# Kernel optimization log

Measured on AMD Instinct MI355X. Metric: run time of the kernel, lower is better.

## Reference

```python
import jax, jax.numpy as jnp
import numpy as np

INPUT_SIZE = 1024
HIDDEN_SIZE = 1024
BATCH = 8192
MLP_H1, MLP_H2 = 16, 8


def _uniform(key, shape, stdv):
    return jax.random.uniform(key, shape, jnp.float32, -stdv, stdv)


def setup_inputs() -> dict:
    key = jax.random.key(0)
    ks = jax.random.split(key, 20)
    stdv = 1.0 / np.sqrt(HIDDEN_SIZE)
    I, H = INPUT_SIZE, HIDDEN_SIZE
    inp = {
        "x": jax.random.normal(ks[0], (BATCH, I), jnp.float32),
        "h": jax.random.normal(ks[1], (BATCH, H), jnp.float32),
        "c": jax.random.normal(ks[2], (BATCH, H), jnp.float32),
        # gate weights (torch layout: matmul(h, W_h*) + matmul(x, W_x*) + b)
        "W_hi": _uniform(ks[3], (H, H), stdv),
        "W_xi": _uniform(ks[4], (I, H), stdv),
        "b_i": _uniform(ks[5], (H,), stdv),
        "W_hc": _uniform(ks[6], (H, H), stdv),
        "W_xc": _uniform(ks[7], (I, H), stdv),
        "b_c": _uniform(ks[8], (H,), stdv),
        "W_ho": _uniform(ks[9], (H, H), stdv),
        "W_xo": _uniform(ks[10], (I, H), stdv),
        "b_o": _uniform(ks[11], (H,), stdv),
        # forget MLP: (I+H) -> 16 -> 8 -> H, ReLU hidden, sigmoid output
        "W1": _uniform(ks[12], (I + H, MLP_H1), stdv),
        "b1": _uniform(ks[13], (MLP_H1,), stdv),
        "W2": _uniform(ks[14], (MLP_H1, MLP_H2), stdv),
        "b2": _uniform(ks[15], (MLP_H2,), stdv),
        "W3": _uniform(ks[16], (MLP_H2, H), stdv),
        "b3": _uniform(ks[17], (H,), stdv),
    }
    return inp


def reference(x, h, c, W_hi, W_xi, b_i, W_hc, W_xc, b_c, W_ho, W_xo, b_o,
              W1, b1, W2, b2, W3, b3):
    # forget gate via small MLP on concat(x, h)
    xh = jnp.concatenate((x, h), axis=1)           # [B, I+H]
    z = jax.nn.relu(xh @ W1 + b1)                  # [B, 16]
    z = jax.nn.relu(z @ W2 + b2)                   # [B, 8]
    f = jax.nn.sigmoid(z @ W3 + b3)                # [B, H]

    i = jax.nn.sigmoid(h @ W_hi + x @ W_xi + b_i)
    g = jnp.tanh(h @ W_hc + x @ W_xc + b_c)
    o = jax.nn.sigmoid(h @ W_ho + x @ W_xo + b_o)

    c_new = f * c + i * g
    h_new = o * jnp.tanh(c_new)
    return (h_new, c_new, f)
```

## Files before the change

kernel.cpp:

```cpp
#include <hip/hip_runtime.h>
#include <math.h>

#define BATCH 8192
#define HDIM  1024
#define KDIM  2048
#define NDIM  3072

typedef __attribute__((ext_vector_type(8))) short short8;
typedef __attribute__((ext_vector_type(4))) float floatx4;

__device__ __forceinline__ float b2f(unsigned short u) {
  union { unsigned int i; float f; } v; v.i = ((unsigned int)u) << 16; return v.f;
}
__device__ __forceinline__ unsigned short f2b(float f) {
  union { unsigned int i; float f; } v; v.f = f;
  unsigned int r = v.i + 0x7FFFu + ((v.i >> 16) & 1u);
  return (unsigned short)(r >> 16);
}
__device__ __forceinline__ float ldsel(const void* p, size_t i, int isbf) {
  return isbf ? b2f(((const unsigned short*)p)[i]) : ((const float*)p)[i];
}
__device__ __forceinline__ float sigf(float x) { return 1.0f / (1.0f + __expf(-x)); }
__device__ __forceinline__ float tanhfast(float x) {
  float a = __builtin_fabsf(x);
  float t = __expf(-2.f * a);
  float r = (1.f - t) / (1.f + t);
  return copysignf(r, x);
}

__device__ __forceinline__ int detect_bf(const void* x) {
  unsigned int w = ((const unsigned int*)x)[threadIdx.x & 63];
  unsigned short lo = (unsigned short)(w & 0xFFFFu);
  int e = (lo >> 7) & 0xFF;
  bool ok = (e >= 110 && e <= 135) || ((lo & 0x7FFFu) == 0);
  unsigned long long m = __ballot(ok);
  return (__popcll(m) >= 48) ? 1 : 0;
}

__device__ __forceinline__ void gld16(const void* g, void* l) {
  auto gp = reinterpret_cast<__attribute__((address_space(1))) unsigned int*>(
      (unsigned long long)g);
  auto lp = reinterpret_cast<__attribute__((address_space(3))) unsigned int*>(
      (unsigned long long)l);
  __builtin_amdgcn_global_load_lds(gp, lp, 16, 0, 0);
}

__device__ __forceinline__ short8 ld8bf(const void* p, size_t off, int isbf) {
  short8 r;
  if (isbf) {
    r = *(const short8*)((const unsigned short*)p + off);
  } else {
    const float* s = (const float*)p + off;
    float4 a = *(const float4*)(s);
    float4 b = *(const float4*)(s + 4);
    r[0]=(short)f2b(a.x); r[1]=(short)f2b(a.y); r[2]=(short)f2b(a.z); r[3]=(short)f2b(a.w);
    r[4]=(short)f2b(b.x); r[5]=(short)f2b(b.y); r[6]=(short)f2b(b.z); r[7]=(short)f2b(b.w);
  }
  return r;
}

__global__ __launch_bounds__(256) void k_all(
    const void* __restrict__ x, const void* __restrict__ h,
    const void* __restrict__ wxi, const void* __restrict__ whi,
    const void* __restrict__ wxc, const void* __restrict__ whc,
    const void* __restrict__ wxo, const void* __restrict__ who,
    const void* __restrict__ W1, const void* __restrict__ b1,
    const void* __restrict__ W2, const void* __restrict__ b2,
    unsigned short* __restrict__ WT, unsigned short* __restrict__ A,
    float* __restrict__ z2) {
  __shared__ __align__(16) char smem[70976];
  const int isbf = detect_bf(x);
  const int bx = blockIdx.x;
  const int tid = threadIdx.x;

  if (bx < 512) {
    unsigned short* lW = (unsigned short*)smem;
    float* part = (float*)(smem + 65536);
    float* z1s  = (float*)(smem + 69888);
    const int m0 = bx * 16;
#pragma unroll
    for (int it = 0; it < 16; ++it) {
      const int chunk = it * 256 + tid;
      const int k = chunk >> 1;
      const int jh = (chunk & 1) * 8;
      unsigned short v[8];
      if (isbf) {
        short8 s = *(const short8*)((const unsigned short*)W1 + (size_t)k * 16 + jh);
#pragma unroll
        for (int j = 0; j < 8; ++j) v[j] = (unsigned short)s[j];
      } else {
        const float* s = (const float*)W1 + (size_t)k * 16 + jh;
        float4 a = *(const float4*)(s);
        float4 b = *(const float4*)(s + 4);
        v[0]=f2b(a.x); v[1]=f2b(a.y); v[2]=f2b(a.z); v[3]=f2b(a.w);
        v[4]=f2b(b.x); v[5]=f2b(b.y); v[6]=f2b(b.z); v[7]=f2b(b.w);
      }
#pragma unroll
      for (int j = 0; j < 8; ++j) {
        const int row = jh + j;
        lW[row * 2048 + (((k >> 3) ^ (row & 7)) << 3) + (k & 7)] = v[j];
      }
    }
    __syncthreads();
    const int w = tid >> 6;
    const int lane = tid & 63;
    const int q = lane >> 4;
    const int r = lane & 15;
    const void* src = (w >> 1) ? h : x;
    const size_t abase = (size_t)(m0 + r) * 1024 + (w & 1) * 512;
    const int kb = (w >> 1) * 1024 + (w & 1) * 512;
    floatx4 acc = {0.f, 0.f, 0.f, 0.f};
#pragma unroll 4
    for (int kt = 0; kt < 16; ++kt) {
      const int kl = kt * 32 + q * 8;
      short8 a = ld8bf(src, abase + kl, isbf);
      const int kg = kb + kl;
      short8 b = *(const short8*)(lW + r * 2048 + (((kg >> 3) ^ (r & 7)) << 3));
      acc = __builtin_amdgcn_mfma_f32_16x16x32_bf16(a, b, acc, 0, 0, 0);
    }
#pragma unroll
    for (int t = 0; t < 4; ++t) part[(w * 16 + q * 4 + t) * 17 + r] = acc[t];
    __syncthreads();
    {
      const int row = tid >> 4;
      const int n = tid & 15;
      float s = part[(0 * 16 + row) * 17 + n] + part[(1 * 16 + row) * 17 + n] +
                part[(2 * 16 + row) * 17 + n] + part[(3 * 16 + row) * 17 + n] +
                ldsel(b1, (size_t)n, isbf);
      z1s[row * 17 + n] = fmaxf(s, 0.f);
    }
    __syncthreads();
    if (tid < 128) {
      const int row = tid >> 3;
      const int p = tid & 7;
      float s = ldsel(b2, (size_t)p, isbf);
#pragma unroll
      for (int nn = 0; nn < 16; ++nn)
        s += z1s[row * 17 + nn] * ldsel(W2, (size_t)nn * 8 + p, isbf);
      z2[(size_t)(m0 + row) * 8 + p] = fmaxf(s, 0.f);
    }
  } else if (bx < 2048) {
    float (*tbuf)[65] = (float(*)[65])smem;
    const int b = bx - 512;
    const int mat = b >> 8;
    const int rem = b & 255;
    const int ti = rem >> 4;
    const int tj = rem & 15;
    const void* Ws[6] = {wxi, whi, wxc, whc, wxo, who};
    const void* W = Ws[mat];
    const int gt = mat >> 1;
    const int half = mat & 1;
    const int rrow = tid >> 3;
    const int c8 = (tid & 7) * 8;
#pragma unroll
    for (int it = 0; it < 2; ++it) {
      int row = it * 32 + rrow;
      size_t off = (size_t)(ti * 64 + row) * 1024 + tj * 64 + c8;
      if (isbf) {
        const unsigned short* s = (const unsigned short*)W + off;
        ushort4 a = *(const ushort4*)(s);
        ushort4 bv = *(const ushort4*)(s + 4);
        tbuf[row][c8+0]=b2f(a.x);  tbuf[row][c8+1]=b2f(a.y);
        tbuf[row][c8+2]=b2f(a.z);  tbuf[row][c8+3]=b2f(a.w);
        tbuf[row][c8+4]=b2f(bv.x); tbuf[row][c8+5]=b2f(bv.y);
        tbuf[row][c8+6]=b2f(bv.z); tbuf[row][c8+7]=b2f(bv.w);
      } else {
        const float* s = (const float*)W + off;
        float4 a = *(const float4*)(s);
        float4 bv = *(const float4*)(s + 4);
        tbuf[row][c8+0]=a.x;  tbuf[row][c8+1]=a.y;  tbuf[row][c8+2]=a.z;  tbuf[row][c8+3]=a.w;
        tbuf[row][c8+4]=bv.x; tbuf[row][c8+5]=bv.y; tbuf[row][c8+6]=bv.z; tbuf[row][c8+7]=bv.w;
      }
    }
    __syncthreads();
#pragma unroll
    for (int it = 0; it < 2; ++it) {
      int nl = it * 32 + rrow;
      int n = gt * 1024 + tj * 64 + nl;
      int kk = half * 1024 + ti * 64 + c8;
      short8 pk;
#pragma unroll
      for (int i = 0; i < 8; ++i) pk[i] = (short)f2b(tbuf[c8 + i][nl]);
      *(short8*)(WT + (size_t)n * KDIM + kk) = pk;
    }
  } else {
    if (isbf) return;
    size_t idx = ((size_t)(bx - 2048) * 256 + tid) * 8;
    int k = (int)(idx & 2047);
    size_t m = idx >> 11;
    const float* s = (k < 1024) ? (const float*)x + m * 1024 + k
                                : (const float*)h + m * 1024 + (k - 1024);
    float4 a = *(const float4*)(s);
    float4 b = *(const float4*)(s + 4);
    short8 pk;
    pk[0]=(short)f2b(a.x); pk[1]=(short)f2b(a.y); pk[2]=(short)f2b(a.z); pk[3]=(short)f2b(a.w);
    pk[4]=(short)f2b(b.x); pk[5]=(short)f2b(b.y); pk[6]=(short)f2b(b.z); pk[7]=(short)f2b(b.w);
    *(short8*)(A + idx) = pk;
  }
}

__global__ __launch_bounds__(256, 3) void k_gemm(
    const void* __restrict__ x, const void* __restrict__ h,
    const unsigned short* __restrict__ Apack,
    const unsigned short* __restrict__ WT,
    unsigned short* __restrict__ P) {
  const int isbf = detect_bf(x);
  const unsigned short* Ax = isbf ? (const unsigned short*)x : Apack;
  const unsigned short* Ah = isbf ? (const unsigned short*)h : (Apack + 1024);
  const int sA = isbf ? 1024 : 2048;
  __shared__ __align__(16) unsigned short lA[128 * 64];
  __shared__ __align__(16) unsigned short lB[128 * 64];
  const int tid = threadIdx.x;
  const int lane = tid & 63;
  const int wv = tid >> 6;
  const int wm = (wv >> 1) << 6;
  const int wn = (wv & 1) << 6;
  const int m0 = blockIdx.y << 7;
  const int n0 = blockIdx.x << 7;

  floatx4 acc[4][4];
  const floatx4 fzero = {0.f, 0.f, 0.f, 0.f};
#pragma unroll
  for (int i = 0; i < 4; ++i)
#pragma unroll
    for (int j = 0; j < 4; ++j) acc[i][j] = fzero;

  int rr[4], kk[4];
#pragma unroll
  for (int ps = 0; ps < 4; ++ps) {
    int chunk = ps * 256 + tid;
    rr[ps] = chunk >> 3;
    kk[ps] = (chunk & 7) ^ (rr[ps] & 7);
  }
  const int px0 = (lane >> 4) ^ (lane & 7);
  const int px1 = ((lane >> 4) + 4) ^ (lane & 7);
  const int rowA = wm + (lane & 15);
  const int rowB = wn + (lane & 15);

  for (int kt = 0; kt < KDIM / 64; ++kt) {
    const int k0 = kt * 64;
    const unsigned short* Abase = (k0 < 1024) ? (Ax + k0) : (Ah + (k0 - 1024));
#pragma unroll
    for (int ps = 0; ps < 4; ++ps) {
      const int chunk = ps * 256 + tid;
      gld16(Abase + (size_t)(m0 + rr[ps]) * sA + kk[ps] * 8, lA + chunk * 8);
      gld16(WT + ((size_t)(n0 + rr[ps]) * KDIM + k0 + kk[ps] * 8), lB + chunk * 8);
    }
    __syncthreads();
#pragma unroll
    for (int s = 0; s < 2; ++s) {
      const int px = s ? px1 : px0;
      short8 af[4], bfr[4];
#pragma unroll
      for (int i = 0; i < 4; ++i)
        af[i] = *(const short8*)(lA + ((((rowA + (i << 4)) << 3) + px) << 3));
#pragma unroll
      for (int i = 0; i < 4; ++i)
        bfr[i] = *(const short8*)(lB + ((((rowB + (i << 4)) << 3) + px) << 3));
#pragma unroll
      for (int mi = 0; mi < 4; ++mi)
#pragma unroll
        for (int ni = 0; ni < 4; ++ni)
          acc[mi][ni] = __builtin_amdgcn_mfma_f32_16x16x32_bf16(
              af[mi], bfr[ni], acc[mi][ni], 0, 0, 0);
    }
    __syncthreads();
  }
  const int col = lane & 15;
  const int rq = (lane >> 4) << 2;
#pragma unroll
  for (int mi = 0; mi < 4; ++mi) {
#pragma unroll
    for (int ni = 0; ni < 4; ++ni) {
      const size_t n = (size_t)(n0 + wn + (ni << 4) + col);
#pragma unroll
      for (int t = 0; t < 4; ++t) {
        const size_t m = (size_t)(m0 + wm + (mi << 4) + rq + t);
        P[m * NDIM + n] = f2b(acc[mi][ni][t]);
      }
    }
  }
}

__global__ __launch_bounds__(256) void k_pointwise(
    const unsigned short* __restrict__ P, const void* __restrict__ x,
    const void* __restrict__ cin,
    const void* __restrict__ bi, const void* __restrict__ bc,
    const void* __restrict__ bo, const float* __restrict__ z2,
    const void* __restrict__ W3, const void* __restrict__ b3,
    void* __restrict__ out) {
  const int isbf = detect_bf(x);
  __shared__ unsigned short w3s[8192];
  const int tid = threadIdx.x;
#pragma unroll
  for (int it = 0; it < 4; ++it) {
    const int idx = (it * 256 + tid) * 8;
    if (isbf) {
      *(short8*)(w3s + idx) = *(const short8*)((const unsigned short*)W3 + idx);
    } else {
      const float* s = (const float*)W3 + idx;
      float4 a = *(const float4*)(s);
      float4 b = *(const float4*)(s + 4);
      short8 pk;
      pk[0]=(short)f2b(a.x); pk[1]=(short)f2b(a.y); pk[2]=(short)f2b(a.z); pk[3]=(short)f2b(a.w);
      pk[4]=(short)f2b(b.x); pk[5]=(short)f2b(b.y); pk[6]=(short)f2b(b.z); pk[7]=(short)f2b(b.w);
      *(short8*)(w3s + idx) = pk;
    }
  }
  __syncthreads();
  const size_t MH = (size_t)BATCH * HDIM;
  const size_t m = blockIdx.x;
  const int n = tid * 4;
  const size_t idx = m * 1024 + n;
  const unsigned short* pr = P + m * NDIM + n;
  ushort4 ui = *(const ushort4*)(pr);
  ushort4 ug = *(const ushort4*)(pr + 1024);
  ushort4 uo = *(const ushort4*)(pr + 2048);
  float pi[4] = {b2f(ui.x), b2f(ui.y), b2f(ui.z), b2f(ui.w)};
  float pg[4] = {b2f(ug.x), b2f(ug.y), b2f(ug.z), b2f(ug.w)};
  float po[4] = {b2f(uo.x), b2f(uo.y), b2f(uo.z), b2f(uo.w)};
  float4 za = *(const float4*)(z2 + m * 8);
  float4 zb = *(const float4*)(z2 + m * 8 + 4);
  float zz[8] = {za.x, za.y, za.z, za.w, zb.x, zb.y, zb.z, zb.w};
  float f3[4];
  float bif[4], bcf[4], bof[4], cf[4];
  if (isbf) {
    ushort4 u3 = *(const ushort4*)((const unsigned short*)b3 + n);
    f3[0]=b2f(u3.x); f3[1]=b2f(u3.y); f3[2]=b2f(u3.z); f3[3]=b2f(u3.w);
    ushort4 a = *(const ushort4*)((const unsigned short*)bi + n);
    ushort4 b = *(const ushort4*)((const unsigned short*)bc + n);
    ushort4 d = *(const ushort4*)((const unsigned short*)bo + n);
    ushort4 e = *(const ushort4*)((const unsigned short*)cin + idx);
    bif[0]=b2f(a.x); bif[1]=b2f(a.y); bif[2]=b2f(a.z); bif[3]=b2f(a.w);
    bcf[0]=b2f(b.x); bcf[1]=b2f(b.y); bcf[2]=b2f(b.z); bcf[3]=b2f(b.w);
    bof[0]=b2f(d.x); bof[1]=b2f(d.y); bof[2]=b2f(d.z); bof[3]=b2f(d.w);
    cf[0]=b2f(e.x);  cf[1]=b2f(e.y);  cf[2]=b2f(e.z);  cf[3]=b2f(e.w);
  } else {
    float4 u3 = *(const float4*)((const float*)b3 + n);
    f3[0]=u3.x; f3[1]=u3.y; f3[2]=u3.z; f3[3]=u3.w;
    float4 a = *(const float4*)((const float*)bi + n);
    float4 b = *(const float4*)((const float*)bc + n);
    float4 d = *(const float4*)((const float*)bo + n);
    float4 e = *(const float4*)((const float*)cin + idx);
    bif[0]=a.x; bif[1]=a.y; bif[2]=a.z; bif[3]=a.w;
    bcf[0]=b.x; bcf[1]=b.y; bcf[2]=b.z; bcf[3]=b.w;
    bof[0]=d.x; bof[1]=d.y; bof[2]=d.z; bof[3]=d.w;
    cf[0]=e.x;  cf[1]=e.y;  cf[2]=e.z;  cf[3]=e.w;
  }
#pragma unroll
  for (int j = 0; j < 8; ++j) {
    const unsigned short* wr = w3s + j * 1024 + n;
    f3[0] += zz[j] * b2f(wr[0]);
    f3[1] += zz[j] * b2f(wr[1]);
    f3[2] += zz[j] * b2f(wr[2]);
    f3[3] += zz[j] * b2f(wr[3]);
  }
  float hn[4], cn[4], ff[4];
#pragma unroll
  for (int t = 0; t < 4; ++t) {
    float F = sigf(f3[t]);
    float I = sigf(pi[t] + bif[t]);
    float G = tanhfast(pg[t] + bcf[t]);
    float O = sigf(po[t] + bof[t]);
    float C = F * cf[t] + I * G;
    ff[t] = F;
    cn[t] = C;
    hn[t] = O * tanhfast(C);
  }
  if (isbf) {
    unsigned short* ob = (unsigned short*)out;
    *(ushort4*)(ob + idx) = make_ushort4(f2b(hn[0]), f2b(hn[1]), f2b(hn[2]), f2b(hn[3]));
    *(ushort4*)(ob + MH + idx) = make_ushort4(f2b(cn[0]), f2b(cn[1]), f2b(cn[2]), f2b(cn[3]));
    *(ushort4*)(ob + 2 * MH + idx) = make_ushort4(f2b(ff[0]), f2b(ff[1]), f2b(ff[2]), f2b(ff[3]));
  } else {
    float* ob = (float*)out;
    *(float4*)(ob + idx) = make_float4(hn[0], hn[1], hn[2], hn[3]);
    *(float4*)(ob + MH + idx) = make_float4(cn[0], cn[1], cn[2], cn[3]);
    *(float4*)(ob + 2 * MH + idx) = make_float4(ff[0], ff[1], ff[2], ff[3]);
  }
}

extern "C" void kernel_launch(void* const* d_in, const int* in_sizes, int n_in,
                              void* d_out, int out_size, void* d_ws, size_t ws_size,
                              hipStream_t stream) {
  const void* x    = d_in[0];
  const void* h    = d_in[1];
  const void* c    = d_in[2];
  const void* W_hi = d_in[3];
  const void* W_xi = d_in[4];
  const void* b_i  = d_in[5];
  const void* W_hc = d_in[6];
  const void* W_xc = d_in[7];
  const void* b_c  = d_in[8];
  const void* W_ho = d_in[9];
  const void* W_xo = d_in[10];
  const void* b_o  = d_in[11];
  const void* W1   = d_in[12];
  const void* b1   = d_in[13];
  const void* W2   = d_in[14];
  const void* b2   = d_in[15];
  const void* W3   = d_in[16];
  const void* b3   = d_in[17];

  char* ws = (char*)d_ws;
  unsigned short* A   = (unsigned short*)ws;
  unsigned short* WT  = (unsigned short*)(ws + 33554432);
  unsigned short* P   = (unsigned short*)(ws + 46137344);
  float*          z2b = (float*)(ws + 96468992);

  k_all<<<dim3(512 + 1536 + 8192), dim3(256), 0, stream>>>(
      x, h, W_xi, W_hi, W_xc, W_hc, W_xo, W_ho, W1, b_i ? b1 : b1, W2, b2,
      WT, A, z2b);
  k_gemm<<<dim3(NDIM / 128, BATCH / 128), dim3(256), 0, stream>>>(x, h, A, WT, P);
  k_pointwise<<<dim3(BATCH), dim3(256), 0, stream>>>(P, x, c, b_i, b_c, b_o,
                                                     z2b, W3, b3, d_out);
}
```

Before: 374.9 us.

## Split fused prep kernel into three kernels and register-cache W3 in pointwise

The monolithic prep kernel, which reserved about 70KB of shared memory for every block, is split into separate kernels for activation packing, weight transpose and the forget-gate MLP. Each can then run at its natural occupancy, and the transpose and packing blocks no longer carry the MLP's large LDS footprint. The pointwise kernel now processes 8 rows per block and keeps W3 and the biases in registers, removing the per-block LDS staging of W3. The costs are extra kernel launches and serialisation between the prep stages, plus higher register pressure in the pointwise kernel.

```diff
diff --git a/kernel.cpp b/kernel.cpp
--- a/kernel.cpp
+++ b/kernel.cpp
@@ -59,135 +59,144 @@
   return r;
 }
 
-__global__ __launch_bounds__(256) void k_all(
+__global__ __launch_bounds__(256) void k_z2(
     const void* __restrict__ x, const void* __restrict__ h,
+    const void* __restrict__ W1, const void* __restrict__ b1,
+    const void* __restrict__ W2, const void* __restrict__ b2,
+    float* __restrict__ z2) {
+  __shared__ __align__(16) char smem[70976];
+  const int isbf = detect_bf(x);
+  const int tid = threadIdx.x;
+  unsigned short* lW = (unsigned short*)smem;
+  float* part = (float*)(smem + 65536);
+  float* z1s  = (float*)(smem + 69888);
+  const int m0 = blockIdx.x * 16;
+#pragma unroll
+  for (int it = 0; it < 16; ++it) {
+    const int chunk = it * 256 + tid;
+    const int k = chunk >> 1;
+    const int jh = (chunk & 1) * 8;
+    unsigned short v[8];
+    if (isbf) {
+      short8 s = *(const short8*)((const unsigned short*)W1 + (size_t)k * 16 + jh);
+#pragma unroll
+      for (int j = 0; j < 8; ++j) v[j] = (unsigned short)s[j];
+    } else {
+      const float* s = (const float*)W1 + (size_t)k * 16 + jh;
+      float4 a = *(const float4*)(s);
+      float4 b = *(const float4*)(s + 4);
+      v[0]=f2b(a.x); v[1]=f2b(a.y); v[2]=f2b(a.z); v[3]=f2b(a.w);
+      v[4]=f2b(b.x); v[5]=f2b(b.y); v[6]=f2b(b.z); v[7]=f2b(b.w);
+    }
+#pragma unroll
+    for (int j = 0; j < 8; ++j) {
+      const int row = jh + j;
+      lW[row * 2048 + (((k >> 3) ^ (row & 7)) << 3) + (k & 7)] = v[j];
+    }
+  }
+  __syncthreads();
+  const int w = tid >> 6;
+  const int lane = tid & 63;
+  const int q = lane >> 4;
+  const int r = lane & 15;
+  const void* src = (w >> 1) ? h : x;
+  const size_t abase = (size_t)(m0 + r) * 1024 + (w & 1) * 512;
+  const int kb = (w >> 1) * 1024 + (w & 1) * 512;
+  floatx4 acc = {0.f, 0.f, 0.f, 0.f};
+#pragma unroll 4
+  for (int kt = 0; kt < 16; ++kt) {
+    const int kl = kt * 32 + q * 8;
+    short8 a = ld8bf(src, abase + kl, isbf);
+    const int kg = kb + kl;
+    short8 b = *(const short8*)(lW + r * 2048 + (((kg >> 3) ^ (r & 7)) << 3));
+    acc = __builtin_amdgcn_mfma_f32_16x16x32_bf16(a, b, acc, 0, 0, 0);
+  }
+#pragma unroll
+  for (int t = 0; t < 4; ++t) part[(w * 16 + q * 4 + t) * 17 + r] = acc[t];
+  __syncthreads();
+  {
+    const int row = tid >> 4;
+    const int n = tid & 15;
+    float s = part[(0 * 16 + row) * 17 + n] + part[(1 * 16 + row) * 17 + n] +
+              part[(2 * 16 + row) * 17 + n] + part[(3 * 16 + row) * 17 + n] +
+              ldsel(b1, (size_t)n, isbf);
+    z1s[row * 17 + n] = fmaxf(s, 0.f);
+  }
+  __syncthreads();
+  if (tid < 128) {
+    const int row = tid >> 3;
+    const int p = tid & 7;
+    float s = ldsel(b2, (size_t)p, isbf);
+#pragma unroll
+    for (int nn = 0; nn < 16; ++nn)
+      s += z1s[row * 17 + nn] * ldsel(W2, (size_t)nn * 8 + p, isbf);
+    z2[(size_t)(m0 + row) * 8 + p] = fmaxf(s, 0.f);
+  }
+}
+
+__global__ __launch_bounds__(256) void k_wt(
+    const void* __restrict__ x,
     const void* __restrict__ wxi, const void* __restrict__ whi,
     const void* __restrict__ wxc, const void* __restrict__ whc,
     const void* __restrict__ wxo, const void* __restrict__ who,
-    const void* __restrict__ W1, const void* __restrict__ b1,
-    const void* __restrict__ W2, const void* __restrict__ b2,
-    unsigned short* __restrict__ WT, unsigned short* __restrict__ A,
-    float* __restrict__ z2) {
-  __shared__ __align__(16) char smem[70976];
+    unsigned short* __restrict__ WT) {
+  __shared__ __align__(16) float tbuf[64][65];
   const int isbf = detect_bf(x);
-  const int bx = blockIdx.x;
   const int tid = threadIdx.x;
-
-  if (bx < 512) {
-    unsigned short* lW = (unsigned short*)smem;
-    float* part = (float*)(smem + 65536);
-    float* z1s  = (float*)(smem + 69888);
-    const int m0 = bx * 16;
-#pragma unroll
-    for (int it = 0; it < 16; ++it) {
-      const int chunk = it * 256 + tid;
-      const int k = chunk >> 1;
-      const int jh = (chunk & 1) * 8;
-      unsigned short v[8];
-      if (isbf) {
-        short8 s = *(const short8*)((const unsigned short*)W1 + (size_t)k * 16 + jh);
-#pragma unroll
-        for (int j = 0; j < 8; ++j) v[j] = (unsigned short)s[j];
-      } else {
-        const float* s = (const float*)W1 + (size_t)k * 16 + jh;
-        float4 a = *(const float4*)(s);
-        float4 b = *(const float4*)(s + 4);
-        v[0]=f2b(a.x); v[1]=f2b(a.y); v[2]=f2b(a.z); v[3]=f2b(a.w);
-        v[4]=f2b(b.x); v[5]=f2b(b.y); v[6]=f2b(b.z); v[7]=f2b(b.w);
-      }
-#pragma unroll
-      for (int j = 0; j < 8; ++j) {
-        const int row = jh + j;
-        lW[row * 2048 + (((k >> 3) ^ (row & 7)) << 3) + (k & 7)] = v[j];
-      }
-    }
-    __syncthreads();
-    const int w = tid >> 6;
-    const int lane = tid & 63;
-    const int q = lane >> 4;
-    const int r = lane & 15;
-    const void* src = (w >> 1) ? h : x;
-    const size_t abase = (size_t)(m0 + r) * 1024 + (w & 1) * 512;
-    const int kb = (w >> 1) * 1024 + (w & 1) * 512;
-    floatx4 acc = {0.f, 0.f, 0.f, 0.f};
-#pragma unroll 4
-    for (int kt = 0; kt < 16; ++kt) {
-      const int kl = kt * 32 + q * 8;
-      short8 a = ld8bf(src, abase + kl, isbf);
-      const int kg = kb + kl;
-      short8 b = *(const short8*)(lW + r * 2048 + (((kg >> 3) ^ (r & 7)) << 3));
-      acc = __builtin_amdgcn_mfma_f32_16x16x32_bf16(a, b, acc, 0, 0, 0);
-    }
-#pragma unroll
-    for (int t = 0; t < 4; ++t) part[(w * 16 + q * 4 + t) * 17 + r] = acc[t];
-    __syncthreads();
-    {
-      const int row = tid >> 4;
-      const int n = tid & 15;
-      float s = part[(0 * 16 + row) * 17 + n] + part[(1 * 16 + row) * 17 + n] +
-                part[(2 * 16 + row) * 17 + n] + part[(3 * 16 + row) * 17 + n] +
-                ldsel(b1, (size_t)n, isbf);
-      z1s[row * 17 + n] = fmaxf(s, 0.f);
-    }
-    __syncthreads();
-    if (tid < 128) {
-      const int row = tid >> 3;
-      const int p = tid & 7;
-      float s = ldsel(b2, (size_t)p, isbf);
-#pragma unroll
-      for (int nn = 0; nn < 16; ++nn)
-        s += z1s[row * 17 + nn] * ldsel(W2, (size_t)nn * 8 + p, isbf);
-      z2[(size_t)(m0 + row) * 8 + p] = fmaxf(s, 0.f);
-    }
-  } else if (bx < 2048) {
-    float (*tbuf)[65] = (float(*)[65])smem;
-    const int b = bx - 512;
-    const int mat = b >> 8;
-    const int rem = b & 255;
-    const int ti = rem >> 4;
-    const int tj = rem & 15;
-    const void* Ws[6] = {wxi, whi, wxc, whc, wxo, who};
-    const void* W = Ws[mat];
-    const int gt = mat >> 1;
-    const int half = mat & 1;
-    const int rrow = tid >> 3;
-    const int c8 = (tid & 7) * 8;
-#pragma unroll
-    for (int it = 0; it < 2; ++it) {
-      int row = it * 32 + rrow;
-      size_t off = (size_t)(ti * 64 + row) * 1024 + tj * 64 + c8;
-      if (isbf) {
-        const unsigned short* s = (const unsigned short*)W + off;
-        ushort4 a = *(const ushort4*)(s);
-        ushort4 bv = *(const ushort4*)(s + 4);
-        tbuf[row][c8+0]=b2f(a.x);  tbuf[row][c8+1]=b2f(a.y);
-        tbuf[row][c8+2]=b2f(a.z);  tbuf[row][c8+3]=b2f(a.w);
-        tbuf[row][c8+4]=b2f(bv.x); tbuf[row][c8+5]=b2f(bv.y);
-        tbuf[row][c8+6]=b2f(bv.z); tbuf[row][c8+7]=b2f(bv.w);
-      } else {
-        const float* s = (const float*)W + off;
-        float4 a = *(const float4*)(s);
-        float4 bv = *(const float4*)(s + 4);
-        tbuf[row][c8+0]=a.x;  tbuf[row][c8+1]=a.y;  tbuf[row][c8+2]=a.z;  tbuf[row][c8+3]=a.w;
-        tbuf[row][c8+4]=bv.x; tbuf[row][c8+5]=bv.y; tbuf[row][c8+6]=bv.z; tbuf[row][c8+7]=bv.w;
-      }
-    }
-    __syncthreads();
-#pragma unroll
-    for (int it = 0; it < 2; ++it) {
-      int nl = it * 32 + rrow;
-      int n = gt * 1024 + tj * 64 + nl;
-      int kk = half * 1024 + ti * 64 + c8;
-      short8 pk;
-#pragma unroll
-      for (int i = 0; i < 8; ++i) pk[i] = (short)f2b(tbuf[c8 + i][nl]);
-      *(short8*)(WT + (size_t)n * KDIM + kk) = pk;
-    }
-  } else {
-    if (isbf) return;
-    size_t idx = ((size_t)(bx - 2048) * 256 + tid) * 8;
-    int k = (int)(idx & 2047);
-    size_t m = idx >> 11;
+  const int b = blockIdx.x;
+  const int mat = b >> 8;
+  const int rem = b & 255;
+  const int ti = rem >> 4;
+  const int tj = rem & 15;
+  const void* Ws[6] = {wxi, whi, wxc, whc, wxo, who};
+  const void* W = Ws[mat];
+  const int gt = mat >> 1;
+  const int half = mat & 1;
+  const int rrow = tid >> 3;
+  const int c8 = (tid & 7) * 8;
+#pragma unroll
+  for (int it = 0; it < 2; ++it) {
+    int row = it * 32 + rrow;
+    size_t off = (size_t)(ti * 64 + row) * 1024 + tj * 64 + c8;
+    if (isbf) {
+      const unsigned short* s = (const unsigned short*)W + off;
+      ushort4 a = *(const ushort4*)(s);
+      ushort4 bv = *(const ushort4*)(s + 4);
+      tbuf[row][c8+0]=b2f(a.x);  tbuf[row][c8+1]=b2f(a.y);
+      tbuf[row][c8+2]=b2f(a.z);  tbuf[row][c8+3]=b2f(a.w);
+      tbuf[row][c8+4]=b2f(bv.x); tbuf[row][c8+5]=b2f(bv.y);
+      tbuf[row][c8+6]=b2f(bv.z); tbuf[row][c8+7]=b2f(bv.w);
+    } else {
+      const float* s = (const float*)W + off;
+      float4 a = *(const float4*)(s);
+      float4 bv = *(const float4*)(s + 4);
+      tbuf[row][c8+0]=a.x;  tbuf[row][c8+1]=a.y;  tbuf[row][c8+2]=a.z;  tbuf[row][c8+3]=a.w;
+      tbuf[row][c8+4]=bv.x; tbuf[row][c8+5]=bv.y; tbuf[row][c8+6]=bv.z; tbuf[row][c8+7]=bv.w;
+    }
+  }
+  __syncthreads();
+#pragma unroll
+  for (int it = 0; it < 2; ++it) {
+    int nl = it * 32 + rrow;
+    int n = gt * 1024 + tj * 64 + nl;
+    int kk = half * 1024 + ti * 64 + c8;
+    short8 pk;
+#pragma unroll
+    for (int i = 0; i < 8; ++i) pk[i] = (short)f2b(tbuf[c8 + i][nl]);
+    *(short8*)(WT + (size_t)n * KDIM + kk) = pk;
+  }
+}
+
+__global__ __launch_bounds__(256) void k_apack(
+    const void* __restrict__ x, const void* __restrict__ h,
+    unsigned short* __restrict__ A) {
+  if (detect_bf(x)) return;
+  const size_t t0 = (size_t)blockIdx.x * 256 + threadIdx.x;
+#pragma unroll
+  for (int it = 0; it < 4; ++it) {
+    const size_t idx = (t0 + (size_t)it * 524288) * 8;
+    const int k = (int)(idx & 2047);
+    const size_t m = idx >> 11;
     const float* s = (k < 1024) ? (const float*)x + m * 1024 + k
                                 : (const float*)h + m * 1024 + (k - 1024);
     float4 a = *(const float4*)(s);
@@ -290,93 +299,95 @@
     const void* __restrict__ W3, const void* __restrict__ b3,
     void* __restrict__ out) {
   const int isbf = detect_bf(x);
-  __shared__ unsigned short w3s[8192];
   const int tid = threadIdx.x;
-#pragma unroll
-  for (int it = 0; it < 4; ++it) {
-    const int idx = (it * 256 + tid) * 8;
-    if (isbf) {
-      *(short8*)(w3s + idx) = *(const short8*)((const unsigned short*)W3 + idx);
-    } else {
-      const float* s = (const float*)W3 + idx;
-      float4 a = *(const float4*)(s);
-      float4 b = *(const float4*)(s + 4);
-      short8 pk;
-      pk[0]=(short)f2b(a.x); pk[1]=(short)f2b(a.y); pk[2]=(short)f2b(a.z); pk[3]=(short)f2b(a.w);
-      pk[4]=(short)f2b(b.x); pk[5]=(short)f2b(b.y); pk[6]=(short)f2b(b.z); pk[7]=(short)f2b(b.w);
-      *(short8*)(w3s + idx) = pk;
-    }
-  }
-  __syncthreads();
+  const int n = tid * 4;
   const size_t MH = (size_t)BATCH * HDIM;
-  const size_t m = blockIdx.x;
-  const int n = tid * 4;
-  const size_t idx = m * 1024 + n;
-  const unsigned short* pr = P + m * NDIM + n;
-  ushort4 ui = *(const ushort4*)(pr);
-  ushort4 ug = *(const ushort4*)(pr + 1024);
-  ushort4 uo = *(const ushort4*)(pr + 2048);
-  float pi[4] = {b2f(ui.x), b2f(ui.y), b2f(ui.z), b2f(ui.w)};
-  float pg[4] = {b2f(ug.x), b2f(ug.y), b2f(ug.z), b2f(ug.w)};
-  float po[4] = {b2f(uo.x), b2f(uo.y), b2f(uo.z), b2f(uo.w)};
-  float4 za = *(const float4*)(z2 + m * 8);
-  float4 zb = *(const float4*)(z2 + m * 8 + 4);
-  float zz[8] = {za.x, za.y, za.z, za.w, zb.x, zb.y, zb.z, zb.w};
-  float f3[4];
-  float bif[4], bcf[4], bof[4], cf[4];
+
+  float w3r[8][4], bif[4], bcf[4], bof[4], b3f[4];
   if (isbf) {
+#pragma unroll
+    for (int j = 0; j < 8; ++j) {
+      ushort4 u = *(const ushort4*)((const unsigned short*)W3 + j * 1024 + n);
+      w3r[j][0]=b2f(u.x); w3r[j][1]=b2f(u.y); w3r[j][2]=b2f(u.z); w3r[j][3]=b2f(u.w);
+    }
     ushort4 u3 = *(const ushort4*)((const unsigned short*)b3 + n);
-    f3[0]=b2f(u3.x); f3[1]=b2f(u3.y); f3[2]=b2f(u3.z); f3[3]=b2f(u3.w);
+    b3f[0]=b2f(u3.x); b3f[1]=b2f(u3.y); b3f[2]=b2f(u3.z); b3f[3]=b2f(u3.w);
     ushort4 a = *(const ushort4*)((const unsigned short*)bi + n);
     ushort4 b = *(const ushort4*)((const unsigned short*)bc + n);
     ushort4 d = *(const ushort4*)((const unsigned short*)bo + n);
-    ushort4 e = *(const ushort4*)((const unsigned short*)cin + idx);
     bif[0]=b2f(a.x); bif[1]=b2f(a.y); bif[2]=b2f(a.z); bif[3]=b2f(a.w);
     bcf[0]=b2f(b.x); bcf[1]=b2f(b.y); bcf[2]=b2f(b.z); bcf[3]=b2f(b.w);
     bof[0]=b2f(d.x); bof[1]=b2f(d.y); bof[2]=b2f(d.z); bof[3]=b2f(d.w);
-    cf[0]=b2f(e.x);  cf[1]=b2f(e.y);  cf[2]=b2f(e.z);  cf[3]=b2f(e.w);
   } else {
+#pragma unroll
+    for (int j = 0; j < 8; ++j) {
+      float4 u = *(const float4*)((const float*)W3 + j * 1024 + n);
+      w3r[j][0]=u.x; w3r[j][1]=u.y; w3r[j][2]=u.z; w3r[j][3]=u.w;
+    }
     float4 u3 = *(const float4*)((const float*)b3 + n);
-    f3[0]=u3.x; f3[1]=u3.y; f3[2]=u3.z; f3[3]=u3.w;
+    b3f[0]=u3.x; b3f[1]=u3.y; b3f[2]=u3.z; b3f[3]=u3.w;
     float4 a = *(const float4*)((const float*)bi + n);
     float4 b = *(const float4*)((const float*)bc + n);
     float4 d = *(const float4*)((const float*)bo + n);
-    float4 e = *(const float4*)((const float*)cin + idx);
     bif[0]=a.x; bif[1]=a.y; bif[2]=a.z; bif[3]=a.w;
     bcf[0]=b.x; bcf[1]=b.y; bcf[2]=b.z; bcf[3]=b.w;
     bof[0]=d.x; bof[1]=d.y; bof[2]=d.z; bof[3]=d.w;
-    cf[0]=e.x;  cf[1]=e.y;  cf[2]=e.z;  cf[3]=e.w;
-  }
-#pragma unroll
-  for (int j = 0; j < 8; ++j) {
-    const unsigned short* wr = w3s + j * 1024 + n;
-    f3[0] += zz[j] * b2f(wr[0]);
-    f3[1] += zz[j] * b2f(wr[1]);
-    f3[2] += zz[j] * b2f(wr[2]);
-    f3[3] += zz[j] * b2f(wr[3]);
-  }
-  float hn[4], cn[4], ff[4];
-#pragma unroll
-  for (int t = 0; t < 4; ++t) {
-    float F = sigf(f3[t]);
-    float I = sigf(pi[t] + bif[t]);
-    float G = tanhfast(pg[t] + bcf[t]);
-    float O = sigf(po[t] + bof[t]);
-    float C = F * cf[t] + I * G;
-    ff[t] = F;
-    cn[t] = C;
-    hn[t] = O * tanhfast(C);
-  }
-  if (isbf) {
-    unsigned short* ob = (unsigned short*)out;
-    *(ushort4*)(ob + idx) = make_ushort4(f2b(hn[0]), f2b(hn[1]), f2b(hn[2]), f2b(hn[3]));
-    *(ushort4*)(ob + MH + idx) = make_ushort4(f2b(cn[0]), f2b(cn[1]), f2b(cn[2]), f2b(cn[3]));
-    *(ushort4*)(ob + 2 * MH + idx) = make_ushort4(f2b(ff[0]), f2b(ff[1]), f2b(ff[2]), f2b(ff[3]));
-  } else {
-    float* ob = (float*)out;
-    *(float4*)(ob + idx) = make_float4(hn[0], hn[1], hn[2], hn[3]);
-    *(float4*)(ob + MH + idx) = make_float4(cn[0], cn[1], cn[2], cn[3]);
-    *(float4*)(ob + 2 * MH + idx) = make_float4(ff[0], ff[1], ff[2], ff[3]);
+  }
+
+  const size_t m0 = (size_t)blockIdx.x * 8;
+#pragma unroll
+  for (int rI = 0; rI < 8; ++rI) {
+    const size_t m = m0 + rI;
+    const size_t idx = m * 1024 + n;
+    const unsigned short* pr = P + m * NDIM + n;
+    ushort4 ui = *(const ushort4*)(pr);
+    ushort4 ug = *(const ushort4*)(pr + 1024);
+    ushort4 uo = *(const ushort4*)(pr + 2048);
+    float pi[4] = {b2f(ui.x), b2f(ui.y), b2f(ui.z), b2f(ui.w)};
+    float pg[4] = {b2f(ug.x), b2f(ug.y), b2f(ug.z), b2f(ug.w)};
+    float po[4] = {b2f(uo.x), b2f(uo.y), b2f(uo.z), b2f(uo.w)};
+    float4 za = *(const float4*)(z2 + m * 8);
+    float4 zb = *(const float4*)(z2 + m * 8 + 4);
+    float zz[8] = {za.x, za.y, za.z, za.w, zb.x, zb.y, zb.z, zb.w};
+    float cf[4];
+    if (isbf) {
+      ushort4 e = *(const ushort4*)((const unsigned short*)cin + idx);
+      cf[0]=b2f(e.x); cf[1]=b2f(e.y); cf[2]=b2f(e.z); cf[3]=b2f(e.w);
+    } else {
+      float4 e = *(const float4*)((const float*)cin + idx);
+      cf[0]=e.x; cf[1]=e.y; cf[2]=e.z; cf[3]=e.w;
+    }
+    float f3[4] = {b3f[0], b3f[1], b3f[2], b3f[3]};
+#pragma unroll
+    for (int j = 0; j < 8; ++j) {
+      f3[0] += zz[j] * w3r[j][0];
+      f3[1] += zz[j] * w3r[j][1];
+      f3[2] += zz[j] * w3r[j][2];
+      f3[3] += zz[j] * w3r[j][3];
+    }
+    float hn[4], cn[4], ff[4];
+#pragma unroll
+    for (int t = 0; t < 4; ++t) {
+      float F = sigf(f3[t]);
+      float I = sigf(pi[t] + bif[t]);
+      float G = tanhfast(pg[t] + bcf[t]);
+      float O = sigf(po[t] + bof[t]);
+      float C = F * cf[t] + I * G;
+      ff[t] = F;
+      cn[t] = C;
+      hn[t] = O * tanhfast(C);
+    }
+    if (isbf) {
+      unsigned short* ob = (unsigned short*)out;
+      *(ushort4*)(ob + idx) = make_ushort4(f2b(hn[0]), f2b(hn[1]), f2b(hn[2]), f2b(hn[3]));
+      *(ushort4*)(ob + MH + idx) = make_ushort4(f2b(cn[0]), f2b(cn[1]), f2b(cn[2]), f2b(cn[3]));
+      *(ushort4*)(ob + 2 * MH + idx) = make_ushort4(f2b(ff[0]), f2b(ff[1]), f2b(ff[2]), f2b(ff[3]));
+    } else {
+      float* ob = (float*)out;
+      *(float4*)(ob + idx) = make_float4(hn[0], hn[1], hn[2], hn[3]);
+      *(float4*)(ob + MH + idx) = make_float4(cn[0], cn[1], cn[2], cn[3]);
+      *(float4*)(ob + 2 * MH + idx) = make_float4(ff[0], ff[1], ff[2], ff[3]);
+    }
   }
 }
 
@@ -408,10 +419,11 @@
   unsigned short* P   = (unsigned short*)(ws + 46137344);
   float*          z2b = (float*)(ws + 96468992);
 
-  k_all<<<dim3(512 + 1536 + 8192), dim3(256), 0, stream>>>(
-      x, h, W_xi, W_hi, W_xc, W_hc, W_xo, W_ho, W1, b_i ? b1 : b1, W2, b2,
-      WT, A, z2b);
+  k_apack<<<dim3(2048), dim3(256), 0, stream>>>(x, h, A);
+  k_wt<<<dim3(1536), dim3(256), 0, stream>>>(x, W_xi, W_hi, W_xc, W_hc,
+                                             W_xo, W_ho, WT);
+  k_z2<<<dim3(512), dim3(256), 0, stream>>>(x, h, W1, b1, W2, b2, z2b);
   k_gemm<<<dim3(NDIM / 128, BATCH / 128), dim3(256), 0, stream>>>(x, h, A, WT, P);
-  k_pointwise<<<dim3(BATCH), dim3(256), 0, stream>>>(P, x, c, b_i, b_c, b_o,
-                                                     z2b, W3, b3, d_out);
-}
+  k_pointwise<<<dim3(BATCH / 8), dim3(256), 0, stream>>>(P, x, c, b_i, b_c, b_o,
+                                                         z2b, W3, b3, d_out);
+}
```

Result: faster. 364.9 us (-2.7%).
